# Kernel optimization log

Hardware: AMD Instinct MI355X
Metric: run time of the kernel (lower is better)

Reference implementation:

```python
import jax, jax.numpy as jnp
import numpy as np

B, N, D = 8, 128, 256
EPS = 1e-5


def _layernorm(x, g, b):
    m = jnp.mean(x, axis=-1, keepdims=True)
    v = jnp.mean(jnp.square(x - m), axis=-1, keepdims=True)
    return (x - m) * jax.lax.rsqrt(v + EPS) * g + b


def setup_inputs() -> dict:
    key = jax.random.key(0)
    ks = jax.random.split(key, 24)
    s = 0.05  # param init scale
    return {
        "text": jax.random.normal(ks[0], (B, N, D), jnp.float32),
        "adj1": jax.random.uniform(ks[1], (B, N, N), jnp.float32),
        "adj2": jax.random.uniform(ks[2], (B, N, N), jnp.float32),
        "edge1": jax.random.normal(ks[3], (B, N, N, D), jnp.float32) * 0.1,
        "edge2": jax.random.normal(ks[4], (B, N, N, D), jnp.float32) * 0.1,
        "textmask": jnp.ones((B, N), jnp.float32),
        "weight": jax.random.normal(ks[5], (D, D), jnp.float32) * s,
        "bias": jax.random.normal(ks[6], (D,), jnp.float32) * s,
        "gamma": jnp.ones((D,), jnp.float32),
        "beta": jnp.zeros((D,), jnp.float32),
        "fuse1_w": jax.random.normal(ks[7], (2 * D, D), jnp.float32) * s,
        "fuse2_w": jax.random.normal(ks[8], (2 * D, D), jnp.float32) * s,
        "fc3_w": jax.random.normal(ks[9], (2 * D, D), jnp.float32) * s,
        "fc1_w0": jax.random.normal(ks[10], (3 * D, D), jnp.float32) * s,
        "fc1_w1": jax.random.normal(ks[11], (D, 1), jnp.float32) * s,
        "fc1_b1": jnp.zeros((1,), jnp.float32),
        "fc2_w0": jax.random.normal(ks[12], (3 * D, D), jnp.float32) * s,
        "fc2_w1": jax.random.normal(ks[13], (D, 1), jnp.float32) * s,
        "fc2_b1": jnp.zeros((1,), jnp.float32),
        "align_lin": jax.random.normal(ks[14], (D, D), jnp.float32) * s,
        "align_bias": jax.random.normal(ks[15], (D,), jnp.float32) * s,
    }


def reference(text, adj1, adj2, edge1, edge2, textmask, weight, bias, gamma,
              beta, fuse1_w, fuse2_w, fc3_w, fc1_w0, fc1_w1, fc1_b1,
              fc2_w0, fc2_w1, fc2_b1, align_lin, align_bias):
    d = text.shape[-1]
    # ---- SelfAlignment ----
    logits = jnp.einsum('bid,bjd->bij', text @ align_lin, text)
    mask_add = (1.0 - textmask)[:, None, :] * -1e20
    probs = jax.nn.softmax(logits + mask_add, axis=-1)
    outss = jnp.einsum('bij,bjd->bid', probs, text) * textmask[..., None] + align_bias

    # ---- GCN body ----
    out = jax.nn.relu(text @ weight)  # [B,N,D]

    # edge contributions are loop-invariant: precompute once
    # torch cat([x,e]) @ W  ==  x @ W[:d] + e @ W[d:]
    e1_fuse = jnp.einsum('bijd,de->bije', edge1, fuse1_w[d:])
    e2_fuse = jnp.einsum('bijd,de->bije', edge2, fuse2_w[d:])
    e1_fc = jnp.einsum('bijd,de->bije', edge1, fc1_w0[2 * d:])
    e2_fc = jnp.einsum('bijd,de->bije', edge2, fc2_w0[2 * d:])

    denom1 = jnp.sum(adj1, axis=2, keepdims=True) + 1.0  # [B,N,1]
    denom2 = jnp.sum(adj2, axis=2, keepdims=True) + 1.0

    for _ in range(3):  # K = 3
        # text1[b,i,j] = out[b,i]; text2[b,i,j] = out[b,j]
        t_i1 = (out @ fc1_w0[:d])[:, :, None, :]        # text1 part, fc1
        t_j1 = (out @ fc1_w0[d:2 * d])[:, None, :, :]   # text2 part, fc1
        t_i2 = (out @ fc2_w0[:d])[:, :, None, :]
        t_j2 = (out @ fc2_w0[d:2 * d])[:, None, :, :]

        teout = jax.nn.relu((out @ fuse1_w[:d])[:, None, :, :] + e1_fuse)  # [B,N,N,D]
        tein = jax.nn.relu((out @ fuse2_w[:d])[:, None, :, :] + e2_fuse)

        s1 = jax.nn.sigmoid(jax.nn.relu(t_i1 + t_j1 + e1_fc) @ fc1_w1 + fc1_b1)[..., 0]  # [B,N,N]
        s2 = jax.nn.sigmoid(jax.nn.relu(t_i2 + t_j2 + e2_fc) @ fc2_w1 + fc2_b1)[..., 0]

        out1 = jnp.einsum('bij,bijd->bid', adj1 * s1, teout) / denom1
        out2 = jnp.einsum('bij,bijd->bid', adj2 * s2, tein) / denom2

        out = jax.nn.relu(out1 @ fc3_w[:d] + out2 @ fc3_w[d:]) + out + bias
        out = _layernorm(out, gamma, beta)  # dropout = identity (eval)
    return out, outss
```

## Files before the change

kernel.cpp:

```cpp
#include <hip/hip_runtime.h>

typedef unsigned short u16;
typedef unsigned int u32;
typedef __attribute__((ext_vector_type(8))) short bf16x8;
typedef __attribute__((ext_vector_type(4))) float f32x4;

__device__ __forceinline__ u16 f2bf(float f) {
  u32 u = __float_as_uint(f);
  return (u16)((u + 0x7fffu + ((u >> 16) & 1u)) >> 16);
}

__device__ __forceinline__ float4 unpack4(const u16* p) {
  uint2 a = *(const uint2*)p;
  float4 r;
  r.x = __uint_as_float(a.x << 16);
  r.y = __uint_as_float(a.x & 0xffff0000u);
  r.z = __uint_as_float(a.y << 16);
  r.w = __uint_as_float(a.y & 0xffff0000u);
  return r;
}

__device__ __forceinline__ void barrier_lgkm() {
  asm volatile("s_waitcnt lgkmcnt(0)" ::: "memory");
  __builtin_amdgcn_s_barrier();
  asm volatile("" ::: "memory");
}

__global__ __launch_bounds__(256) void gemm_edge(
    const float* __restrict__ Af, const u16* __restrict__ Bt,
    u16* __restrict__ E) {
  __shared__ __align__(16) u16 Asm[2][8192];
  const int tid = threadIdx.x, lane = tid & 63, w = tid >> 6;
  const int m = lane & 15, q = lane >> 4;
  const int p = blockIdx.x;
  const int rt = (p & 7) * 128 + (p >> 5);
  const int ct = (p >> 3) & 3;
  const int wrow = (w & 1) * 64, wcol = (w >> 1) * 64;
  const float* Ab = Af + (long)rt * 32768;
  const char* Bb = (const char*)Bt + (long)ct * 65536;
  const int r0 = tid >> 4, c4 = (tid & 15) * 4;
  f32x4 acc[4][4];
#pragma unroll
  for (int r = 0; r < 4; ++r)
#pragma unroll
    for (int c = 0; c < 4; ++c) acc[r][c] = (f32x4){0.f, 0.f, 0.f, 0.f};

  float4 pre[8];
#pragma unroll
  for (int it = 0; it < 8; ++it)
    pre[it] = *(const float4*)(Ab + (long)(it * 16 + r0) * 256 + c4);

#pragma unroll
  for (int kc = 0; kc < 4; ++kc) {
    char* As = (char*)Asm[kc & 1];
#pragma unroll
    for (int it = 0; it < 8; ++it) {
      int r = it * 16 + r0;
      ushort4 h;
      h.x = f2bf(pre[it].x); h.y = f2bf(pre[it].y);
      h.z = f2bf(pre[it].z); h.w = f2bf(pre[it].w);
      *(ushort4*)(As + r * 128 + ((c4 * 2) ^ ((r & 7) * 16))) = h;
    }
    if (kc < 3) {
#pragma unroll
      for (int it = 0; it < 8; ++it)
        pre[it] = *(const float4*)(Ab + (long)(it * 16 + r0) * 256 +
                                   (kc + 1) * 64 + c4);
    }
    barrier_lgkm();
#pragma unroll
    for (int s = 0; s < 2; ++s) {
      const int ko2 = (s * 32 + q * 8) * 2;
      bf16x8 av[4], bv[4];
#pragma unroll
      for (int c = 0; c < 4; ++c) {
        int col = wcol + c * 16 + m;
        bv[c] = *(const bf16x8*)(Bb + kc * 16384 + col * 128 +
                                 (ko2 ^ ((col & 7) * 16)));
      }
#pragma unroll
      for (int r = 0; r < 4; ++r) {
        int row = wrow + r * 16 + m;
        av[r] = *(const bf16x8*)(As + row * 128 + (ko2 ^ ((row & 7) * 16)));
      }
#pragma unroll
      for (int r = 0; r < 4; ++r)
#pragma unroll
        for (int c = 0; c < 4; ++c)
          acc[r][c] = __builtin_amdgcn_mfma_f32_16x16x32_bf16(
              av[r], bv[c], acc[r][c], 0, 0, 0);
    }
  }
#pragma unroll
  for (int r = 0; r < 4; ++r)
#pragma unroll
    for (int c = 0; c < 4; ++c)
#pragma unroll
      for (int g = 0; g < 4; ++g) {
        long gr = (long)rt * 128 + wrow + r * 16 + q * 4 + g;
        int gc = ct * 128 + wcol + c * 16 + m;
        E[gr * 512 + gc] = f2bf(acc[r][c][g]);
      }
}

template<int K, int RF, int CF, bool OUT_BF16, bool RELU0, bool SUM2>
__global__ __launch_bounds__(256) void gemm_mfma(
    const float* __restrict__ A, const u16* __restrict__ Bt,
    void* __restrict__ Cv, int Ntot, float* __restrict__ relu_dst,
    const float* __restrict__ A2) {
  constexpr int ROWS = RF * 16;
  constexpr int LD = 72;
  __shared__ __align__(16) u16 Asm[2][ROWS * LD];
  const int tid = threadIdx.x;
  const int lane = tid & 63;
  const int w = tid >> 6;
  const int m = lane & 15;
  const int q = lane >> 4;
  const int wcol = w * (CF * 16);
  const long rowbase = (long)blockIdx.x * ROWS;
  const long colbase = (long)blockIdx.y * (CF * 64);
  const int r0 = tid >> 4, c4 = (tid & 15) * 4;
  f32x4 acc[RF][CF];
#pragma unroll
  for (int r = 0; r < RF; ++r)
#pragma unroll
    for (int c = 0; c < CF; ++c) acc[r][c] = (f32x4){0.f, 0.f, 0.f, 0.f};

  float4 pre[RF], pre2[RF];
#pragma unroll
  for (int it = 0; it < RF; ++it) {
    pre[it] = *(const float4*)(A + (rowbase + it * 16 + r0) * K + c4);
    if constexpr (SUM2)
      pre2[it] = *(const float4*)(A2 + (rowbase + it * 16 + r0) * K + c4);
  }

#pragma unroll
  for (int kc = 0; kc < K / 64; ++kc) {
    u16* As = (u16*)Asm[kc & 1];
#pragma unroll
    for (int it = 0; it < RF; ++it) {
      float4 v = pre[it];
      if constexpr (SUM2) {
        v.x += pre2[it].x; v.y += pre2[it].y;
        v.z += pre2[it].z; v.w += pre2[it].w;
      }
      ushort4 h;
      h.x = f2bf(v.x); h.y = f2bf(v.y); h.z = f2bf(v.z); h.w = f2bf(v.w);
      *(ushort4*)&As[(it * 16 + r0) * LD + c4] = h;
    }
    if (kc + 1 < K / 64) {
#pragma unroll
      for (int it = 0; it < RF; ++it) {
        pre[it] = *(const float4*)(A + (rowbase + it * 16 + r0) * K +
                                   (kc + 1) * 64 + c4);
        if constexpr (SUM2)
          pre2[it] = *(const float4*)(A2 + (rowbase + it * 16 + r0) * K +
                                      (kc + 1) * 64 + c4);
      }
    }
    barrier_lgkm();
#pragma unroll
    for (int s = 0; s < 2; ++s) {
      const int ko = s * 32 + q * 8;
      bf16x8 av[RF], bv[CF];
#pragma unroll
      for (int c = 0; c < CF; ++c)
        bv[c] = *(const bf16x8*)(Bt + (long)(colbase + wcol + c * 16 + m) * K +
                                 kc * 64 + ko);
#pragma unroll
      for (int r = 0; r < RF; ++r)
        av[r] = *(const bf16x8*)&As[(r * 16 + m) * LD + ko];
#pragma unroll
      for (int r = 0; r < RF; ++r)
#pragma unroll
        for (int c = 0; c < CF; ++c)
          acc[r][c] = __builtin_amdgcn_mfma_f32_16x16x32_bf16(
              av[r], bv[c], acc[r][c], 0, 0, 0);
    }
  }
#pragma unroll
  for (int r = 0; r < RF; ++r)
#pragma unroll
    for (int c = 0; c < CF; ++c)
#pragma unroll
      for (int g = 0; g < 4; ++g) {
        long gr = rowbase + r * 16 + q * 4 + g;
        long gc = colbase + wcol + c * 16 + m;
        float v = acc[r][c][g];
        if constexpr (OUT_BF16) ((u16*)Cv)[gr * Ntot + gc] = f2bf(v);
        else                    ((float*)Cv)[gr * Ntot + gc] = v;
        if constexpr (RELU0) {
          if (gc < 256) relu_dst[gr * 256 + gc] = fmaxf(v, 0.f);
        }
      }
}

__global__ __launch_bounds__(256) void prep_bt(
    const float* __restrict__ weight, const float* __restrict__ align_lin,
    const float* __restrict__ fuse1_w, const float* __restrict__ fuse2_w,
    const float* __restrict__ fc1_w0, const float* __restrict__ fc2_w0,
    const float* __restrict__ fc3_w,
    u16* BtE1, u16* BtE2, u16* BtW0, u16* BtLoop, u16* BtFc3) {
  int g = blockIdx.x * 256 + threadIdx.x;
  if (g < 262144) {
    int t = g & 131071;
    int col = t >> 8, k = t & 255;
    float v;
    if (g < 131072)
      v = (col < 256) ? fuse1_w[(256 + k) * 256 + col]
                      : fc1_w0[(512 + k) * 256 + (col - 256)];
    else
      v = (col < 256) ? fuse2_w[(256 + k) * 256 + col]
                      : fc2_w0[(512 + k) * 256 + (col - 256)];
    int ct = col >> 7, cc = col & 127, kc = k >> 6, kk = k & 63;
    u16* dst = (g < 131072) ? BtE1 : BtE2;
    dst[ct * 32768 + kc * 8192 + cc * 64 + (kk ^ ((cc & 7) * 8))] = f2bf(v);
  } else if (g < 393216) {
    int t = g - 262144;
    int c = t >> 8, k = t & 255;
    float v = (c < 256) ? weight[k * 256 + c] : align_lin[k * 256 + (c - 256)];
    BtW0[t] = f2bf(v);
  } else if (g < 786432) {
    int t = g - 393216;
    int c = t >> 8, k = t & 255;
    int seg = c >> 8, cc = c & 255;
    float v;
    if      (seg == 0) v = fuse1_w[k * 256 + cc];
    else if (seg == 1) v = fuse2_w[k * 256 + cc];
    else if (seg == 2) v = fc1_w0[k * 256 + cc];
    else if (seg == 3) v = fc1_w0[(256 + k) * 256 + cc];
    else if (seg == 4) v = fc2_w0[k * 256 + cc];
    else               v = fc2_w0[(256 + k) * 256 + cc];
    BtLoop[t] = f2bf(v);
  } else {
    int t = g - 786432;
    int c = t >> 9, k = t & 511;
    BtFc3[t] = f2bf(fc3_w[k * 256 + c]);
  }
}

__global__ __launch_bounds__(128) void align_kernel(
    const float* __restrict__ text, const float* __restrict__ T0,
    const float* __restrict__ textmask, const float* __restrict__ align_bias,
    float* __restrict__ outss) {
  const int bi = blockIdx.x;
  const int b = bi >> 7;
  const int tid = threadIdx.x;
  __shared__ float ta[256];
  __shared__ float pr[128];
  __shared__ float red[128];
  ta[tid]       = T0[(long)bi * 512 + 256 + tid];
  ta[tid + 128] = T0[(long)bi * 512 + 384 + tid];
  __syncthreads();
  const float* trow = text + (long)(b * 128 + tid) * 256;
  float dot = 0.f;
  for (int d = 0; d < 256; d += 4) {
    float4 t4 = *(const float4*)(trow + d);
    dot += t4.x * ta[d] + t4.y * ta[d + 1] + t4.z * ta[d + 2] + t4.w * ta[d + 3];
  }
  float logit = dot + (1.0f - textmask[b * 128 + tid]) * -1e20f;
  pr[tid] = logit;
  red[tid] = logit;
  __syncthreads();
  for (int off = 64; off; off >>= 1) {
    if (tid < off) red[tid] = fmaxf(red[tid], red[tid + off]);
    __syncthreads();
  }
  float mx = red[0];
  __syncthreads();
  float e = __expf(pr[tid] - mx);
  red[tid] = e;
  __syncthreads();
  for (int off = 64; off; off >>= 1) {
    if (tid < off) red[tid] += red[tid + off];
    __syncthreads();
  }
  float inv = 1.0f / red[0];
  __syncthreads();
  pr[tid] = e * inv;
  __syncthreads();
  const float mi = textmask[bi];
  for (int h = 0; h < 2; ++h) {
    int d = tid + h * 128;
    float s = 0.f;
    for (int j = 0; j < 128; ++j)
      s += pr[j] * text[(long)(b * 128 + j) * 256 + d];
    outss[(long)bi * 256 + d] = s * mi + align_bias[d];
  }
}

__global__ __launch_bounds__(256) void fused_gate(
    const u16* __restrict__ E1, const u16* __restrict__ E2,
    const float* __restrict__ P, const float* __restrict__ adj1,
    const float* __restrict__ adj2, const float* __restrict__ fc1w1,
    const float* __restrict__ fc1b1, const float* __restrict__ fc2w1,
    const float* __restrict__ fc2b1, float* __restrict__ OUa,
    float* __restrict__ OUb) {
  const int tid = threadIdx.x, lane = tid & 63, w = tid >> 6;
  const int bi = blockIdx.x >> 1, half = blockIdx.x & 1;
  const int b = bi >> 7;
  const int d4 = lane * 4;
  const long rowi = (long)bi * 1536;
  const long ebase = (long)bi * 65536;
  const int abase = bi * 128;
  float* __restrict__ OU = half ? OUb : OUa;

  __shared__ float sA[64], sB[64];
  __shared__ float redA[4][256], redB[4][256];
  __shared__ float dInv[2];

  if (tid < 64) sA[tid] = adj1[abase + half * 64 + tid];
  else if (tid < 128) sB[tid - 64] = adj2[abase + half * 64 + (tid - 64)];
  if (w == 0) {
    float v = adj1[abase + lane] + adj1[abase + 64 + lane];
#pragma unroll
    for (int off = 32; off; off >>= 1) v += __shfl_xor(v, off);
    if (lane == 0) dInv[0] = 1.f / (1.f + v);
  } else if (w == 1) {
    float v = adj2[abase + lane] + adj2[abase + 64 + lane];
#pragma unroll
    for (int off = 32; off; off >>= 1) v += __shfl_xor(v, off);
    if (lane == 0) dInv[1] = 1.f / (1.f + v);
  }
  __syncthreads();

  const float4 ti1 = *(const float4*)(P + rowi + 512 + d4);
  const float4 ti2 = *(const float4*)(P + rowi + 1024 + d4);
  const float4 w1v = *(const float4*)(fc1w1 + d4);
  const float4 w2v = *(const float4*)(fc2w1 + d4);
  const float b1 = fc1b1[0], b2 = fc2b1[0];

  float4 acc1 = {0.f, 0.f, 0.f, 0.f}, acc2 = {0.f, 0.f, 0.f, 0.f};

#pragma unroll 2
  for (int t = 0; t < 16; ++t) {
    const int jl = w * 16 + t;
    const int j = half * 64 + jl;
    const long er = ebase + (long)j * 512;
    const long rowj = (long)((b << 7) + j) * 1536;
    float4 e1c = unpack4(E1 + er + 256 + d4);
    float4 e2c = unpack4(E2 + er + 256 + d4);
    float4 t1 = *(const float4*)(P + rowj + 768 + d4);
    float4 t2 = *(const float4*)(P + rowj + 1280 + d4);
    float z1 = fmaxf(ti1.x + t1.x + e1c.x, 0.f) * w1v.x +
               fmaxf(ti1.y + t1.y + e1c.y, 0.f) * w1v.y +
               fmaxf(ti1.z + t1.z + e1c.z, 0.f) * w1v.z +
               fmaxf(ti1.w + t1.w + e1c.w, 0.f) * w1v.w;
    float z2 = fmaxf(ti2.x + t2.x + e2c.x, 0.f) * w2v.x +
               fmaxf(ti2.y + t2.y + e2c.y, 0.f) * w2v.y +
               fmaxf(ti2.z + t2.z + e2c.z, 0.f) * w2v.z +
               fmaxf(ti2.w + t2.w + e2c.w, 0.f) * w2v.w;
#pragma unroll
    for (int off = 1; off < 64; off <<= 1) {
      z1 += __shfl_xor(z1, off);
      z2 += __shfl_xor(z2, off);
    }
    float s1 = sA[jl] * __builtin_amdgcn_rcpf(1.f + __expf(-(z1 + b1)));
    float s2 = sB[jl] * __builtin_amdgcn_rcpf(1.f + __expf(-(z2 + b2)));
    float4 e1f = unpack4(E1 + er + d4);
    float4 e2f = unpack4(E2 + er + d4);
    float4 o1 = *(const float4*)(P + rowj + d4);
    float4 o2 = *(const float4*)(P + rowj + 256 + d4);
    acc1.x += s1 * fmaxf(o1.x + e1f.x, 0.f);
    acc1.y += s1 * fmaxf(o1.y + e1f.y, 0.f);
    acc1.z += s1 * fmaxf(o1.z + e1f.z, 0.f);
    acc1.w += s1 * fmaxf(o1.w + e1f.w, 0.f);
    acc2.x += s2 * fmaxf(o2.x + e2f.x, 0.f);
    acc2.y += s2 * fmaxf(o2.y + e2f.y, 0.f);
    acc2.z += s2 * fmaxf(o2.z + e2f.z, 0.f);
    acc2.w += s2 * fmaxf(o2.w + e2f.w, 0.f);
  }

  *(float4*)&redA[w][d4] = acc1;
  *(float4*)&redB[w][d4] = acc2;
  __syncthreads();
  float r1 = redA[0][tid] + redA[1][tid] + redA[2][tid] + redA[3][tid];
  float r2 = redB[0][tid] + redB[1][tid] + redB[2][tid] + redB[3][tid];
  OU[(long)bi * 512 + tid] = r1 * dInv[0];
  OU[(long)bi * 512 + 256 + tid] = r2 * dInv[1];
}

__global__ __launch_bounds__(256) void ln_kernel(
    const float* __restrict__ Y, const float* __restrict__ prev,
    const float* __restrict__ bias, const float* __restrict__ gamma,
    const float* __restrict__ beta, float* __restrict__ dst) {
  const int row = blockIdx.x, tid = threadIdx.x, lane = tid & 63, w = tid >> 6;
  const long idx = (long)row * 256 + tid;
  float v = fmaxf(Y[idx], 0.f) + prev[idx] + bias[tid];
  float s = v;
#pragma unroll
  for (int off = 32; off; off >>= 1) s += __shfl_xor(s, off);
  __shared__ float wsA[4], wsB[4];
  if (lane == 0) wsA[w] = s;
  __syncthreads();
  float mean = (wsA[0] + wsA[1] + wsA[2] + wsA[3]) * (1.0f / 256.0f);
  float c = v - mean;
  float s2 = c * c;
#pragma unroll
  for (int off = 32; off; off >>= 1) s2 += __shfl_xor(s2, off);
  if (lane == 0) wsB[w] = s2;
  __syncthreads();
  float var = (wsB[0] + wsB[1] + wsB[2] + wsB[3]) * (1.0f / 256.0f);
  dst[idx] = c * rsqrtf(var + 1e-5f) * gamma[tid] + beta[tid];
}

extern "C" void kernel_launch(void* const* d_in, const int* in_sizes, int n_in,
                              void* d_out, int out_size, void* d_ws, size_t ws_size,
                              hipStream_t stream) {
  const float* text      = (const float*)d_in[0];
  const float* adj1      = (const float*)d_in[1];
  const float* adj2      = (const float*)d_in[2];
  const float* edge1     = (const float*)d_in[3];
  const float* edge2     = (const float*)d_in[4];
  const float* textmask  = (const float*)d_in[5];
  const float* weight    = (const float*)d_in[6];
  const float* bias      = (const float*)d_in[7];
  const float* gamma     = (const float*)d_in[8];
  const float* beta      = (const float*)d_in[9];
  const float* fuse1_w   = (const float*)d_in[10];
  const float* fuse2_w   = (const float*)d_in[11];
  const float* fc3_w     = (const float*)d_in[12];
  const float* fc1_w0    = (const float*)d_in[13];
  const float* fc1_w1    = (const float*)d_in[14];
  const float* fc1_b1    = (const float*)d_in[15];
  const float* fc2_w0    = (const float*)d_in[16];
  const float* fc2_w1    = (const float*)d_in[17];
  const float* fc2_b1    = (const float*)d_in[18];
  const float* align_lin = (const float*)d_in[19];
  const float* align_bias= (const float*)d_in[20];
  float* outF = (float*)d_out;

  char* w8 = (char*)d_ws;
  u16* E1   = (u16*)(w8 + 67108864);
  u16* E2   = (u16*)(w8 + 201326592);
  u16* BtE1 = (u16*)(w8 + 335544320);
  u16* BtE2 = BtE1 + 131072;
  u16* BtW0 = BtE2 + 131072;
  u16* BtLoop = BtW0 + 131072;
  u16* BtFc3  = BtLoop + 393216;
  float* P    = (float*)w8;
  float* T0   = P + 1572864;
  float* OUa  = T0 + 524288;
  float* OUb  = OUa + 524288;
  float* outb = OUb + 524288;
  float* Yb   = outb + 262144;

  prep_bt<<<3584, 256, 0, stream>>>(weight, align_lin, fuse1_w, fuse2_w,
                                    fc1_w0, fc2_w0, fc3_w,
                                    BtE1, BtE2, BtW0, BtLoop, BtFc3);
  gemm_edge<<<4096, 256, 0, stream>>>(edge1, BtE1, E1);
  gemm_edge<<<4096, 256, 0, stream>>>(edge2, BtE2, E2);
  gemm_mfma<256, 2, 2, false, true, false><<<dim3(32, 4), 256, 0, stream>>>(
      text, BtW0, T0, 512, outb, nullptr);
  align_kernel<<<1024, 128, 0, stream>>>(text, T0, textmask, align_bias,
                                         outF + 262144);
  for (int it = 0; it < 3; ++it) {
    gemm_mfma<256, 2, 2, false, false, false><<<dim3(32, 12), 256, 0, stream>>>(
        outb, BtLoop, P, 1536, nullptr, nullptr);
    fused_gate<<<2048, 256, 0, stream>>>(E1, E2, P, adj1, adj2, fc1_w1, fc1_b1,
                                         fc2_w1, fc2_b1, OUa, OUb);
    gemm_mfma<512, 1, 2, false, false, true><<<dim3(64, 2), 256, 0, stream>>>(
        OUa, BtFc3, Yb, 256, nullptr, OUb);
    ln_kernel<<<1024, 256, 0, stream>>>(Yb, outb, bias, gamma, beta,
                                        (it == 2) ? outF : outb);
  }
}
```

Measured before the change: 737.9 us.

## Make edge GEMM persistent with LDS-resident weight tile and async loads

The edge projection GEMM now launches 256 persistent blocks of 512 threads. Each block loads its 128-column weight slice once into LDS using global_load_lds and then loops over 16 row tiles. A two-deep register prefetch of the fp32 A operand overlaps the next K-chunk loads with the MFMA work. This removes the repeated global weight reads and the per-tile launch overhead of the old 4096-block grid. In exchange, LDS use rises to about 96KB per block, occupancy falls, and the tile loop runs serially within each block.

```diff
diff --git a/kernel.cpp b/kernel.cpp
--- a/kernel.cpp
+++ b/kernel.cpp
@@ -20,87 +20,110 @@
   return r;
 }
 
+__device__ __forceinline__ void glds16(const void* g, void* l) {
+  __builtin_amdgcn_global_load_lds(
+      (const __attribute__((address_space(1))) unsigned int*)g,
+      (__attribute__((address_space(3))) unsigned int*)l, 16, 0, 0);
+}
+
 __device__ __forceinline__ void barrier_lgkm() {
   asm volatile("s_waitcnt lgkmcnt(0)" ::: "memory");
   __builtin_amdgcn_s_barrier();
   asm volatile("" ::: "memory");
 }
 
-__global__ __launch_bounds__(256) void gemm_edge(
+__global__ __launch_bounds__(512) void gemm_edge(
     const float* __restrict__ Af, const u16* __restrict__ Bt,
     u16* __restrict__ E) {
+  __shared__ __align__(16) u16 Bsm[32768];
   __shared__ __align__(16) u16 Asm[2][8192];
   const int tid = threadIdx.x, lane = tid & 63, w = tid >> 6;
   const int m = lane & 15, q = lane >> 4;
-  const int p = blockIdx.x;
-  const int rt = (p & 7) * 128 + (p >> 5);
-  const int ct = (p >> 3) & 3;
-  const int wrow = (w & 1) * 64, wcol = (w >> 1) * 64;
-  const float* Ab = Af + (long)rt * 32768;
+  const int bid = blockIdx.x;
+  const int grp = (bid & 7) * 8 + (bid >> 5);
+  const int ct = (bid >> 3) & 3;
+  const int wrow = (w & 1) * 64, wcol = (w >> 1) * 32;
   const char* Bb = (const char*)Bt + (long)ct * 65536;
-  const int r0 = tid >> 4, c4 = (tid & 15) * 4;
-  f32x4 acc[4][4];
+  const int r0 = tid >> 2;
+  const int cq = (tid & 3) * 16;
+
+#pragma unroll
+  for (int it = 0; it < 8; ++it)
+    glds16(Bb + it * 8192 + tid * 16, (char*)Bsm + it * 8192 + tid * 16);
+
+  const float* A0 = Af + (long)grp * 16 * 32768;
+  float4 pre[2][4];
+#pragma unroll
+  for (int it = 0; it < 4; ++it) {
+    pre[0][it] = *(const float4*)(A0 + (long)r0 * 256 + cq + it * 4);
+    pre[1][it] = *(const float4*)(A0 + (long)r0 * 256 + 64 + cq + it * 4);
+  }
+  f32x4 acc[4][2];
 #pragma unroll
   for (int r = 0; r < 4; ++r)
 #pragma unroll
-    for (int c = 0; c < 4; ++c) acc[r][c] = (f32x4){0.f, 0.f, 0.f, 0.f};
-
-  float4 pre[8];
-#pragma unroll
-  for (int it = 0; it < 8; ++it)
-    pre[it] = *(const float4*)(Ab + (long)(it * 16 + r0) * 256 + c4);
-
-#pragma unroll
-  for (int kc = 0; kc < 4; ++kc) {
-    char* As = (char*)Asm[kc & 1];
-#pragma unroll
-    for (int it = 0; it < 8; ++it) {
-      int r = it * 16 + r0;
-      ushort4 h;
-      h.x = f2bf(pre[it].x); h.y = f2bf(pre[it].y);
-      h.z = f2bf(pre[it].z); h.w = f2bf(pre[it].w);
-      *(ushort4*)(As + r * 128 + ((c4 * 2) ^ ((r & 7) * 16))) = h;
+    for (int c = 0; c < 2; ++c) acc[r][c] = (f32x4){0.f, 0.f, 0.f, 0.f};
+
+  for (int t = 0; t < 16; ++t) {
+#pragma unroll
+    for (int kc = 0; kc < 4; ++kc) {
+      char* As = (char*)Asm[kc & 1];
+#pragma unroll
+      for (int it = 0; it < 4; ++it) {
+        float4 v = pre[kc & 1][it];
+        ushort4 h;
+        h.x = f2bf(v.x); h.y = f2bf(v.y); h.z = f2bf(v.z); h.w = f2bf(v.w);
+        int cb = (cq + it * 4) * 2;
+        *(ushort4*)(As + r0 * 128 + (cb ^ ((r0 & 7) * 16))) = h;
+      }
+      {
+        int kc2 = (kc + 2) & 3, t2 = t + ((kc + 2) >> 2);
+        if (t2 < 16) {
+          const float* An = A0 + (long)t2 * 32768;
+#pragma unroll
+          for (int it = 0; it < 4; ++it)
+            pre[kc & 1][it] =
+                *(const float4*)(An + (long)r0 * 256 + kc2 * 64 + cq + it * 4);
+        }
+      }
+      barrier_lgkm();
+#pragma unroll
+      for (int s = 0; s < 2; ++s) {
+        const int ko2 = (s * 32 + q * 8) * 2;
+        bf16x8 av[4], bv[2];
+#pragma unroll
+        for (int c = 0; c < 2; ++c) {
+          int col = wcol + c * 16 + m;
+          bv[c] = *(const bf16x8*)((const char*)Bsm + kc * 16384 + col * 128 +
+                                   (ko2 ^ ((col & 7) * 16)));
+        }
+#pragma unroll
+        for (int r = 0; r < 4; ++r) {
+          int row = wrow + r * 16 + m;
+          av[r] = *(const bf16x8*)(As + row * 128 + (ko2 ^ ((row & 7) * 16)));
+        }
+#pragma unroll
+        for (int r = 0; r < 4; ++r)
+#pragma unroll
+          for (int c = 0; c < 2; ++c)
+            acc[r][c] = __builtin_amdgcn_mfma_f32_16x16x32_bf16(
+                av[r], bv[c], acc[r][c], 0, 0, 0);
+      }
     }
-    if (kc < 3) {
-#pragma unroll
-      for (int it = 0; it < 8; ++it)
-        pre[it] = *(const float4*)(Ab + (long)(it * 16 + r0) * 256 +
-                                   (kc + 1) * 64 + c4);
-    }
-    barrier_lgkm();
-#pragma unroll
-    for (int s = 0; s < 2; ++s) {
-      const int ko2 = (s * 32 + q * 8) * 2;
-      bf16x8 av[4], bv[4];
-#pragma unroll
-      for (int c = 0; c < 4; ++c) {
-        int col = wcol + c * 16 + m;
-        bv[c] = *(const bf16x8*)(Bb + kc * 16384 + col * 128 +
-                                 (ko2 ^ ((col & 7) * 16)));
-      }
-#pragma unroll
-      for (int r = 0; r < 4; ++r) {
-        int row = wrow + r * 16 + m;
-        av[r] = *(const bf16x8*)(As + row * 128 + (ko2 ^ ((row & 7) * 16)));
-      }
-#pragma unroll
-      for (int r = 0; r < 4; ++r)
-#pragma unroll
-        for (int c = 0; c < 4; ++c)
-          acc[r][c] = __builtin_amdgcn_mfma_f32_16x16x32_bf16(
-              av[r], bv[c], acc[r][c], 0, 0, 0);
-    }
-  }
-#pragma unroll
-  for (int r = 0; r < 4; ++r)
-#pragma unroll
-    for (int c = 0; c < 4; ++c)
-#pragma unroll
-      for (int g = 0; g < 4; ++g) {
-        long gr = (long)rt * 128 + wrow + r * 16 + q * 4 + g;
-        int gc = ct * 128 + wcol + c * 16 + m;
-        E[gr * 512 + gc] = f2bf(acc[r][c][g]);
-      }
+    const long grow = (long)(grp * 16 + t) * 128;
+#pragma unroll
+    for (int r = 0; r < 4; ++r)
+#pragma unroll
+      for (int c = 0; c < 2; ++c) {
+#pragma unroll
+        for (int g = 0; g < 4; ++g) {
+          long gr = grow + wrow + r * 16 + q * 4 + g;
+          int gc = ct * 128 + wcol + c * 16 + m;
+          E[gr * 512 + gc] = f2bf(acc[r][c][g]);
+        }
+        acc[r][c] = (f32x4){0.f, 0.f, 0.f, 0.f};
+      }
+  }
 }
 
 template<int K, int RF, int CF, bool OUT_BF16, bool RELU0, bool SUM2>
@@ -448,8 +471,8 @@
   prep_bt<<<3584, 256, 0, stream>>>(weight, align_lin, fuse1_w, fuse2_w,
                                     fc1_w0, fc2_w0, fc3_w,
                                     BtE1, BtE2, BtW0, BtLoop, BtFc3);
-  gemm_edge<<<4096, 256, 0, stream>>>(edge1, BtE1, E1);
-  gemm_edge<<<4096, 256, 0, stream>>>(edge2, BtE2, E2);
+  gemm_edge<<<256, 512, 0, stream>>>(edge1, BtE1, E1);
+  gemm_edge<<<256, 512, 0, stream>>>(edge2, BtE2, E2);
   gemm_mfma<256, 2, 2, false, true, false><<<dim3(32, 4), 256, 0, stream>>>(
       text, BtW0, T0, 512, outb, nullptr);
   align_kernel<<<1024, 128, 0, stream>>>(text, T0, textmask, align_bias,
```

Result: faster. 713.2 us (-3.3%).

## Make edge GEMM persistent with LDS-resident weight slice and cross-tile prefetch

Applied to the files above, without the earlier changes.

The edge GEMM now launches 512 blocks instead of 4096. Each block loads its full 128-column weight slice (64KB bf16) into LDS once via global_load_lds, then loops over 8 row tiles. The A-tile fp32 prefetch carries across tile boundaries so loads overlap the previous tile's MFMAs, and the A buffer becomes single-buffered with an extra barrier. This removes repeated per-block B loads and launch overhead, at the cost of much larger LDS use (about 80KB per block), which lowers occupancy, and fewer blocks to spread over the CUs.

```diff
diff --git a/kernel.cpp b/kernel.cpp
--- a/kernel.cpp
+++ b/kernel.cpp
@@ -20,87 +20,122 @@
   return r;
 }
 
+__device__ __forceinline__ void glds16(const void* g, void* l) {
+  __builtin_amdgcn_global_load_lds(
+      (const __attribute__((address_space(1))) unsigned int*)g,
+      (__attribute__((address_space(3))) unsigned int*)l, 16, 0, 0);
+}
+
 __device__ __forceinline__ void barrier_lgkm() {
   asm volatile("s_waitcnt lgkmcnt(0)" ::: "memory");
   __builtin_amdgcn_s_barrier();
   asm volatile("" ::: "memory");
 }
+__device__ __forceinline__ void barrier_plain() {
+  asm volatile("" ::: "memory");
+  __builtin_amdgcn_s_barrier();
+  asm volatile("" ::: "memory");
+}
 
 __global__ __launch_bounds__(256) void gemm_edge(
     const float* __restrict__ Af, const u16* __restrict__ Bt,
     u16* __restrict__ E) {
-  __shared__ __align__(16) u16 Asm[2][8192];
+  __shared__ __align__(16) u16 Bsm[32768];
+  __shared__ __align__(16) u16 Asm[8192];
   const int tid = threadIdx.x, lane = tid & 63, w = tid >> 6;
   const int m = lane & 15, q = lane >> 4;
-  const int p = blockIdx.x;
-  const int rt = (p & 7) * 128 + (p >> 5);
-  const int ct = (p >> 3) & 3;
+  const int b = blockIdx.x;
+  const int x = b & 7, v = b >> 3;
+  const int cs = v & 3;
+  const int rg = x * 16 + (v >> 2);
   const int wrow = (w & 1) * 64, wcol = (w >> 1) * 64;
-  const float* Ab = Af + (long)rt * 32768;
-  const char* Bb = (const char*)Bt + (long)ct * 65536;
-  const int r0 = tid >> 4, c4 = (tid & 15) * 4;
+  const char* Bb = (const char*)Bt + (long)cs * 65536;
+
+#pragma unroll
+  for (int i = 0; i < 16; ++i)
+    glds16(Bb + i * 4096 + tid * 16, (char*)Bsm + i * 4096 + tid * 16);
+  __syncthreads();
+
+  const int sr = w * 32 + (lane >> 3);
+  const int sc = (lane & 7) * 8;
+  const int slot = (lane & 7) * 16;
+
+  const float* Ab0 = Af + (long)rg * 8 * 32768;
+  float4 pa[4], pb[4];
+#pragma unroll
+  for (int i = 0; i < 4; ++i) {
+    const float* src = Ab0 + (long)(sr + i * 8) * 256 + sc;
+    pa[i] = *(const float4*)src;
+    pb[i] = *(const float4*)(src + 4);
+  }
+
   f32x4 acc[4][4];
-#pragma unroll
-  for (int r = 0; r < 4; ++r)
-#pragma unroll
-    for (int c = 0; c < 4; ++c) acc[r][c] = (f32x4){0.f, 0.f, 0.f, 0.f};
-
-  float4 pre[8];
-#pragma unroll
-  for (int it = 0; it < 8; ++it)
-    pre[it] = *(const float4*)(Ab + (long)(it * 16 + r0) * 256 + c4);
-
-#pragma unroll
-  for (int kc = 0; kc < 4; ++kc) {
-    char* As = (char*)Asm[kc & 1];
-#pragma unroll
-    for (int it = 0; it < 8; ++it) {
-      int r = it * 16 + r0;
-      ushort4 h;
-      h.x = f2bf(pre[it].x); h.y = f2bf(pre[it].y);
-      h.z = f2bf(pre[it].z); h.w = f2bf(pre[it].w);
-      *(ushort4*)(As + r * 128 + ((c4 * 2) ^ ((r & 7) * 16))) = h;
+  for (int t = 0; t < 8; ++t) {
+    const float* Ab = Ab0 + (long)t * 32768;
+#pragma unroll
+    for (int r = 0; r < 4; ++r)
+#pragma unroll
+      for (int c = 0; c < 4; ++c) acc[r][c] = (f32x4){0.f, 0.f, 0.f, 0.f};
+#pragma unroll
+    for (int kc = 0; kc < 4; ++kc) {
+      barrier_plain();
+#pragma unroll
+      for (int i = 0; i < 4; ++i) {
+        int row = sr + i * 8;
+        uint4 st;
+        st.x = (u32)f2bf(pa[i].x) | ((u32)f2bf(pa[i].y) << 16);
+        st.y = (u32)f2bf(pa[i].z) | ((u32)f2bf(pa[i].w) << 16);
+        st.z = (u32)f2bf(pb[i].x) | ((u32)f2bf(pb[i].y) << 16);
+        st.w = (u32)f2bf(pb[i].z) | ((u32)f2bf(pb[i].w) << 16);
+        *(uint4*)((char*)Asm + row * 128 + (slot ^ ((row & 7) * 16))) = st;
+      }
+      if (kc < 3 || t < 7) {
+        const int kc2 = (kc + 1) & 3;
+        const float* An = (kc < 3) ? Ab : (Ab + 32768);
+#pragma unroll
+        for (int i = 0; i < 4; ++i) {
+          const float* src = An + (long)(sr + i * 8) * 256 + kc2 * 64 + sc;
+          pa[i] = *(const float4*)src;
+          pb[i] = *(const float4*)(src + 4);
+        }
+      }
+      barrier_lgkm();
+#pragma unroll
+      for (int s = 0; s < 2; ++s) {
+        const int ko2 = (s * 32 + q * 8) * 2;
+        bf16x8 av[4], bv[4];
+#pragma unroll
+        for (int r = 0; r < 4; ++r) {
+          int row = wrow + r * 16 + m;
+          av[r] = *(const bf16x8*)((char*)Asm + row * 128 +
+                                   (ko2 ^ ((row & 7) * 16)));
+        }
+#pragma unroll
+        for (int c = 0; c < 4; ++c) {
+          int col = wcol + c * 16 + m;
+          bv[c] = *(const bf16x8*)((char*)Bsm + kc * 16384 + col * 128 +
+                                   (ko2 ^ ((col & 7) * 16)));
+        }
+#pragma unroll
+        for (int r = 0; r < 4; ++r)
+#pragma unroll
+          for (int c = 0; c < 4; ++c)
+            acc[r][c] = __builtin_amdgcn_mfma_f32_16x16x32_bf16(
+                av[r], bv[c], acc[r][c], 0, 0, 0);
+      }
     }
-    if (kc < 3) {
-#pragma unroll
-      for (int it = 0; it < 8; ++it)
-        pre[it] = *(const float4*)(Ab + (long)(it * 16 + r0) * 256 +
-                                   (kc + 1) * 64 + c4);
-    }
-    barrier_lgkm();
-#pragma unroll
-    for (int s = 0; s < 2; ++s) {
-      const int ko2 = (s * 32 + q * 8) * 2;
-      bf16x8 av[4], bv[4];
-#pragma unroll
-      for (int c = 0; c < 4; ++c) {
-        int col = wcol + c * 16 + m;
-        bv[c] = *(const bf16x8*)(Bb + kc * 16384 + col * 128 +
-                                 (ko2 ^ ((col & 7) * 16)));
-      }
-#pragma unroll
-      for (int r = 0; r < 4; ++r) {
-        int row = wrow + r * 16 + m;
-        av[r] = *(const bf16x8*)(As + row * 128 + (ko2 ^ ((row & 7) * 16)));
-      }
-#pragma unroll
-      for (int r = 0; r < 4; ++r)
-#pragma unroll
-        for (int c = 0; c < 4; ++c)
-          acc[r][c] = __builtin_amdgcn_mfma_f32_16x16x32_bf16(
-              av[r], bv[c], acc[r][c], 0, 0, 0);
-    }
-  }
-#pragma unroll
-  for (int r = 0; r < 4; ++r)
-#pragma unroll
-    for (int c = 0; c < 4; ++c)
-#pragma unroll
-      for (int g = 0; g < 4; ++g) {
-        long gr = (long)rt * 128 + wrow + r * 16 + q * 4 + g;
-        int gc = ct * 128 + wcol + c * 16 + m;
-        E[gr * 512 + gc] = f2bf(acc[r][c][g]);
-      }
+    const long grow = (long)(rg * 8 + t) * 128;
+#pragma unroll
+    for (int r = 0; r < 4; ++r)
+#pragma unroll
+      for (int c = 0; c < 4; ++c)
+#pragma unroll
+        for (int g = 0; g < 4; ++g) {
+          long gr = grow + wrow + r * 16 + q * 4 + g;
+          int gc = cs * 128 + wcol + c * 16 + m;
+          E[gr * 512 + gc] = f2bf(acc[r][c][g]);
+        }
+  }
 }
 
 template<int K, int RF, int CF, bool OUT_BF16, bool RELU0, bool SUM2>
@@ -448,8 +483,8 @@
   prep_bt<<<3584, 256, 0, stream>>>(weight, align_lin, fuse1_w, fuse2_w,
                                     fc1_w0, fc2_w0, fc3_w,
                                     BtE1, BtE2, BtW0, BtLoop, BtFc3);
-  gemm_edge<<<4096, 256, 0, stream>>>(edge1, BtE1, E1);
-  gemm_edge<<<4096, 256, 0, stream>>>(edge2, BtE2, E2);
+  gemm_edge<<<512, 256, 0, stream>>>(edge1, BtE1, E1);
+  gemm_edge<<<512, 256, 0, stream>>>(edge2, BtE2, E2);
   gemm_mfma<256, 2, 2, false, true, false><<<dim3(32, 4), 256, 0, stream>>>(
       text, BtW0, T0, 512, outb, nullptr);
   align_kernel<<<1024, 128, 0, stream>>>(text, T0, textmask, align_bias,
```

After: 706.2 us. 4.3% less time.
